# Kernel optimization log

Measured on AMD Instinct MI355X. Metric: run time of the kernel, lower is better.

## Reference

```python
import jax, jax.numpy as jnp
import numpy as np

DIM = 128      # token feature dim
HEADS = 4
HEAD_DIM = DIM // HEADS
H = 512
W = 512
NSP = 4096     # n_spixels = H*W/scale
TEMP = DIM ** (-0.5)   # NOTE: original scales by full-dim ** -0.5
NEG = -9.0e15
EPS = 1e-12    # torch F.normalize eps


def setup_inputs() -> dict:
    key = jax.random.key(0)
    k1, k2, k3, k4 = jax.random.split(key, 4)
    return {
        "spf": jax.random.normal(k1, (DIM, NSP), jnp.float32),
        "segments": jax.random.randint(k2, (H, W), 0, NSP, jnp.int32),
        "w_qkv": jax.random.normal(k3, (DIM, 3 * DIM), jnp.float32) / np.sqrt(DIM),
        "w_out": jax.random.normal(k4, (DIM, DIM), jnp.float32) / np.sqrt(DIM),
        "b_out": jnp.zeros((DIM,), jnp.float32),
    }


def build_adjacency(seg, n_sp):
    """Vectorized version of get_A: for every 2x2 window (i in [0,h-3], j in [0,w-3])
    connect the max and min superpixel labels; zero the diagonal."""
    a = seg[:-2, :-2]
    b = seg[:-2, 1:-1]
    c = seg[1:-1, :-2]
    d = seg[1:-1, 1:-1]
    mx = jnp.maximum(jnp.maximum(a, b), jnp.maximum(c, d)).ravel()
    mn = jnp.minimum(jnp.minimum(a, b), jnp.minimum(c, d)).ravel()
    A = jnp.zeros((n_sp, n_sp), jnp.float32)
    A = A.at[mx, mn].set(1.0)
    A = A.at[mn, mx].set(1.0)
    # fill_diagonal(A, 0) (also removes windows where max == min)
    A = A * (1.0 - jnp.eye(n_sp, dtype=jnp.float32))
    return A


def _l2norm(t):
    n = jnp.sqrt(jnp.sum(t * t, axis=-1, keepdims=True))
    return t / jnp.maximum(n, EPS)


def reference(spf, segments, w_qkv, w_out, b_out):
    A = build_adjacency(segments, NSP)                      # [n, n]
    x = spf.T                                               # [n, dim]
    qkv = x @ w_qkv                                         # [n, 3*dim]
    q, k, v = jnp.split(qkv, 3, axis=-1)
    split = lambda t: t.reshape(NSP, HEADS, HEAD_DIM).transpose(1, 0, 2)  # [h, n, d]
    q, k, v = split(q), split(k), split(v)
    q = _l2norm(q)
    k = _l2norm(k)
    # Original masks per-head scores, then keeps only head 0's attention
    # (attn[0][0]) and broadcasts it over all heads' v. We compute only
    # head 0's scores (mathematically identical output).
    scores = (q[0] @ k[0].T) * TEMP                         # [n, n] cosine scores
    scores = jnp.where(A > 0, scores, NEG)
    eye = jnp.eye(NSP, dtype=bool)
    scores = jnp.where(eye, 1.0, scores)                    # np.fill_diagonal(attn, 1)
    attn = jax.nn.softmax(scores, axis=-1)                  # [n, n]
    out = jnp.einsum('nm,hmd->hnd', attn, v)                # shared attn over heads
    out = out.transpose(1, 0, 2).reshape(NSP, DIM)          # [n, dim]
    out = out @ w_out + b_out                               # to_out Linear
    # map_sp2p: scatter superpixel features back to pixel grid (hard assignment)
    pix = out[segments]                                     # [H, W, dim]
    return pix.transpose(2, 0, 1)[None]                     # [1, dim, H, W]
```

## Files before the change

### kernel.cpp

```cpp
#include <hip/hip_runtime.h>

#define NSP 4096
#define HW 512
#define TEMP 0.08838834764831845f
#define MAXE 640
#define ADJ_BLOCKS 1017
#define GEMM_BLOCKS 256

__global__ void __launch_bounds__(256) adj_qkv(
    const int* __restrict__ seg, unsigned int* __restrict__ mask,
    const float* __restrict__ spf, const float* __restrict__ wqkv,
    const float* __restrict__ wout,
    float* __restrict__ Q0, float* __restrict__ K0, float* __restrict__ V) {
    __shared__ float xs[128][16];
    __shared__ float vrs[16][128];
    int t = threadIdx.x;
    if (blockIdx.x < ADJ_BLOCKS) {
        int idx = blockIdx.x * 256 + t;
        if (idx >= 510 * 510) return;
        int i = idx / 510, j = idx - i * 510;
        const int* r = seg + i * HW + j;
        int a = r[0], b = r[1], c = r[HW], d = r[HW + 1];
        int mx = max(max(a, b), max(c, d));
        int mn = min(min(a, b), min(c, d));
        if (mx == mn) return;
        atomicOr(&mask[mx * 128 + (mn >> 5)], 1u << (mn & 31));
        atomicOr(&mask[mn * 128 + (mx >> 5)], 1u << (mx & 31));
        return;
    }
    int nbase = (blockIdx.x - ADJ_BLOCKS) * 16;
#pragma unroll
    for (int i = 0; i < 8; ++i) {
        int idx = t + 256 * i;
        int d = idx >> 4, nn = idx & 15;
        xs[d][nn] = spf[d * NSP + nbase + nn];
    }
    __syncthreads();
    int n = t >> 4, k = t & 15;
    int ng = nbase + n;
    const float* wq = (k < 8) ? (wqkv + k * 4) : (wqkv + 96 + k * 4);
    const float* wv1 = wqkv + 256 + 4 * k;
    const float* wv2 = wqkv + 256 + 64 + 4 * k;
    float4 a0 = {0.f,0.f,0.f,0.f}, a1 = {0.f,0.f,0.f,0.f}, a2 = {0.f,0.f,0.f,0.f};
#pragma unroll 4
    for (int d = 0; d < 128; ++d) {
        float x = xs[d][n];
        float4 wa = *(const float4*)(wq  + d * 384);
        float4 wb = *(const float4*)(wv1 + d * 384);
        float4 wc = *(const float4*)(wv2 + d * 384);
        a0.x += x * wa.x; a0.y += x * wa.y; a0.z += x * wa.z; a0.w += x * wa.w;
        a1.x += x * wb.x; a1.y += x * wb.y; a1.z += x * wb.z; a1.w += x * wb.w;
        a2.x += x * wc.x; a2.y += x * wc.y; a2.z += x * wc.z; a2.w += x * wc.w;
    }
    float s = a0.x * a0.x + a0.y * a0.y + a0.z * a0.z + a0.w * a0.w;
    s += __shfl_xor(s, 1);
    s += __shfl_xor(s, 2);
    s += __shfl_xor(s, 4);
    float inv = 1.0f / fmaxf(sqrtf(s), 1e-12f);
    a0.x *= inv; a0.y *= inv; a0.z *= inv; a0.w *= inv;
    float* qk = (k < 8) ? (Q0 + ng * 32 + k * 4) : (K0 + ng * 32 + (k - 8) * 4);
    *(float4*)qk = a0;
    *(float4*)&vrs[n][4 * k] = a1;
    *(float4*)&vrs[n][64 + 4 * k] = a2;
    __syncthreads();
    float4 c1 = {0.f,0.f,0.f,0.f}, c2 = {0.f,0.f,0.f,0.f};
#pragma unroll 4
    for (int d = 0; d < 128; ++d) {
        float v = vrs[n][d];
        float4 w1 = *(const float4*)(wout + d * 128 + 4 * k);
        float4 w2 = *(const float4*)(wout + d * 128 + 64 + 4 * k);
        c1.x += v * w1.x; c1.y += v * w1.y; c1.z += v * w1.z; c1.w += v * w1.w;
        c2.x += v * w2.x; c2.y += v * w2.y; c2.z += v * w2.z; c2.w += v * w2.w;
    }
    *(float4*)(V + ng * 128 + 4 * k) = c1;
    *(float4*)(V + ng * 128 + 64 + 4 * k) = c2;
}

__global__ void __launch_bounds__(256) sparse_attn(
    const unsigned int* __restrict__ mask, const float* __restrict__ Q0,
    const float* __restrict__ K0, const float* __restrict__ V,
    const float* __restrict__ bout, float* __restrict__ fin) {
    __shared__ unsigned int words[4][128];
    __shared__ int   pfx[4][128];
    __shared__ int   midx[4][MAXE];
    __shared__ float wts[4][MAXE];
    __shared__ float q0s[4][32];
    int t = threadIdx.x, lane = t & 63, w = t >> 6;
    int n = blockIdx.x * 4 + w;

    uint2 mw = ((const uint2*)(mask + n * 128))[lane];
    ((uint2*)words[w])[lane] = mw;
    int pc1 = __popc(mw.y);
    int p = __popc(mw.x) + pc1;
#pragma unroll
    for (int off = 1; off < 64; off <<= 1) {
        int y = __shfl_up(p, off);
        if (lane >= off) p += y;
    }
    pfx[w][2 * lane + 1] = p;
    pfx[w][2 * lane]     = p - pc1;
    int E = min(__shfl(p, 63), MAXE);
    if (lane < 32) q0s[w][lane] = Q0[n * 32 + lane];
    __syncthreads();

    for (int e = lane; e < E; e += 64) {
        int lo = 0, hi = 127;
        while (lo < hi) { int mid = (lo + hi) >> 1; if (pfx[w][mid] > e) hi = mid; else lo = mid + 1; }
        int base = lo ? pfx[w][lo - 1] : 0;
        int r = e - base;
        unsigned int x = words[w][lo];
        for (int i = 0; i < r; ++i) x &= x - 1;
        int m = lo * 32 + (__ffs(x) - 1);
        const float4* kp = (const float4*)(K0 + m * 32);
        float s = 0.f;
#pragma unroll
        for (int i = 0; i < 8; ++i) {
            float4 kv = kp[i];
            s += q0s[w][4 * i + 0] * kv.x + q0s[w][4 * i + 1] * kv.y +
                 q0s[w][4 * i + 2] * kv.z + q0s[w][4 * i + 3] * kv.w;
        }
        wts[w][e]  = __expf(s * TEMP - 1.0f);
        midx[w][e] = m;
    }
    __syncthreads();

    int cgc = lane & 31, eg = lane >> 5;
    const float4* V4 = (const float4*)V;
    float4 acc = {0.f,0.f,0.f,0.f};
    float wp = 0.f;
    int e = eg;
    for (; e + 2 < E; e += 4) {
        float wa = wts[w][e];     int ma = midx[w][e];
        float wb = wts[w][e + 2]; int mb = midx[w][e + 2];
        float4 va = V4[ma * 32 + cgc];
        float4 vb = V4[mb * 32 + cgc];
        acc.x += wa * va.x + wb * vb.x;
        acc.y += wa * va.y + wb * vb.y;
        acc.z += wa * va.z + wb * vb.z;
        acc.w += wa * va.w + wb * vb.w;
        wp += wa + wb;
    }
    for (; e < E; e += 2) {
        float wt = wts[w][e];
        float4 v = V4[midx[w][e] * 32 + cgc];
        acc.x += wt * v.x; acc.y += wt * v.y; acc.z += wt * v.z; acc.w += wt * v.w;
        wp += wt;
    }
    acc.x += __shfl_xor(acc.x, 32);
    acc.y += __shfl_xor(acc.y, 32);
    acc.z += __shfl_xor(acc.z, 32);
    acc.w += __shfl_xor(acc.w, 32);
    wp    += __shfl_xor(wp, 32);
    if (lane < 32) {
        float4 vd = V4[n * 32 + cgc];
        float4 bb = ((const float4*)bout)[cgc];
        float inv = 1.0f / (1.0f + wp);
        float4 o;
        o.x = (acc.x + vd.x) * inv + bb.x;
        o.y = (acc.y + vd.y) * inv + bb.y;
        o.z = (acc.z + vd.z) * inv + bb.z;
        o.w = (acc.w + vd.w) * inv + bb.w;
        ((float4*)fin)[n * 32 + cgc] = o;
    }
}

#define GOUT_PIX 256
#define GOUT_CH  32
__global__ void __launch_bounds__(256) gather_out(
    const float* __restrict__ fin, const int* __restrict__ seg,
    float* __restrict__ out) {
    __shared__ __align__(16) float tile[GOUT_CH][260];
    __shared__ int sseg[GOUT_PIX];
    int t = threadIdx.x;
    int pixbase = (blockIdx.x >> 2) * GOUT_PIX;
    int cbase = (blockIdx.x & 3) * GOUT_CH;

    sseg[t] = seg[pixbase + t];
    __syncthreads();

    const float4* f4 = (const float4*)fin;
    int c8 = t & 7;
    int pp = t >> 3;
#pragma unroll
    for (int i = 0; i < 8; ++i) {
        int p = pp + 32 * i;
        float4 v = f4[sseg[p] * 32 + (cbase >> 2) + c8];
        tile[4 * c8 + 0][p] = v.x;
        tile[4 * c8 + 1][p] = v.y;
        tile[4 * c8 + 2][p] = v.z;
        tile[4 * c8 + 3][p] = v.w;
    }
    __syncthreads();

    int wv = t >> 6, lane = t & 63;
#pragma unroll
    for (int s = 0; s < 8; ++s) {
        int ch = wv * 8 + s;
        float4 v = *(const float4*)&tile[ch][4 * lane];
        *(float4*)(out + (size_t)(cbase + ch) * (HW * HW) + pixbase + 4 * lane) = v;
    }
}

extern "C" void kernel_launch(void* const* d_in, const int* in_sizes, int n_in,
                              void* d_out, int out_size, void* d_ws, size_t ws_size,
                              hipStream_t stream) {
    const float* spf  = (const float*)d_in[0];
    const int*   seg  = (const int*)d_in[1];
    const float* wqkv = (const float*)d_in[2];
    const float* wout = (const float*)d_in[3];
    const float* bout = (const float*)d_in[4];
    float* out = (float*)d_out;

    char* ws = (char*)d_ws;
    unsigned int* mask = (unsigned int*)ws;
    float* Q0  = (float*)(ws + 0x200000);
    float* K0  = (float*)(ws + 0x280000);
    float* V   = (float*)(ws + 0x300000);
    float* fin = (float*)(ws + 0x500000);

    hipMemsetAsync(mask, 0, 2u << 20, stream);
    hipLaunchKernelGGL(adj_qkv, dim3(ADJ_BLOCKS + GEMM_BLOCKS), dim3(256), 0, stream,
                       seg, mask, spf, wqkv, wout, Q0, K0, V);
    hipLaunchKernelGGL(sparse_attn, dim3(1024), dim3(256), 0, stream,
                       mask, Q0, K0, V, bout, fin);
    hipLaunchKernelGGL(gather_out, dim3((HW * HW) / GOUT_PIX * 4), dim3(256), 0, stream,
                       fin, seg, out);
}
```

Before: 230.3 us.

## Use one block per superpixel row with atomic edge compaction in sparse attention

Sparse attention now launches one 128-thread block per row instead of one wavefront per row. Each thread scans a single mask word and appends its neighbour indices through an LDS atomic counter, which replaces the prefix-sum, binary-search and bit-peeling edge enumeration. Score computation and V accumulation are spread over 128 threads, and the partial sums are reduced through shared memory. Edge order becomes nondeterministic, so floating-point summation order can vary between runs, and the extra block syncs add per-row overhead.

Result: no change. 226.1 us (-1.8%).

```diff
diff --git a/kernel.cpp b/kernel.cpp
--- a/kernel.cpp
+++ b/kernel.cpp
@@ -76,91 +76,84 @@
     *(float4*)(V + ng * 128 + 64 + 4 * k) = c2;
 }
 
-__global__ void __launch_bounds__(256) sparse_attn(
+__global__ void __launch_bounds__(128) sparse_attn(
     const unsigned int* __restrict__ mask, const float* __restrict__ Q0,
     const float* __restrict__ K0, const float* __restrict__ V,
     const float* __restrict__ bout, float* __restrict__ fin) {
-    __shared__ unsigned int words[4][128];
-    __shared__ int   pfx[4][128];
-    __shared__ int   midx[4][MAXE];
-    __shared__ float wts[4][MAXE];
-    __shared__ float q0s[4][32];
-    int t = threadIdx.x, lane = t & 63, w = t >> 6;
-    int n = blockIdx.x * 4 + w;
-
-    uint2 mw = ((const uint2*)(mask + n * 128))[lane];
-    ((uint2*)words[w])[lane] = mw;
-    int pc1 = __popc(mw.y);
-    int p = __popc(mw.x) + pc1;
-#pragma unroll
-    for (int off = 1; off < 64; off <<= 1) {
-        int y = __shfl_up(p, off);
-        if (lane >= off) p += y;
-    }
-    pfx[w][2 * lane + 1] = p;
-    pfx[w][2 * lane]     = p - pc1;
-    int E = min(__shfl(p, 63), MAXE);
-    if (lane < 32) q0s[w][lane] = Q0[n * 32 + lane];
-    __syncthreads();
-
-    for (int e = lane; e < E; e += 64) {
-        int lo = 0, hi = 127;
-        while (lo < hi) { int mid = (lo + hi) >> 1; if (pfx[w][mid] > e) hi = mid; else lo = mid + 1; }
-        int base = lo ? pfx[w][lo - 1] : 0;
-        int r = e - base;
-        unsigned int x = words[w][lo];
-        for (int i = 0; i < r; ++i) x &= x - 1;
-        int m = lo * 32 + (__ffs(x) - 1);
+    int n = blockIdx.x;
+    int t = threadIdx.x;
+    __shared__ int   midx[MAXE];
+    __shared__ float wts[MAXE];
+    __shared__ float q0s[32];
+    __shared__ float4 redv[4][32];
+    __shared__ float  redw[4];
+    __shared__ int ecnt;
+
+    unsigned int w = mask[n * 128 + t];
+    if (t == 0) ecnt = 0;
+    if (t < 32) q0s[t] = Q0[n * 32 + t];
+    __syncthreads();
+
+    while (w) {
+        int b = __ffs(w) - 1;
+        w &= w - 1;
+        int pos = atomicAdd(&ecnt, 1);
+        if (pos < MAXE) midx[pos] = t * 32 + b;
+    }
+    __syncthreads();
+    int E = min(ecnt, MAXE);
+
+    for (int e = t; e < E; e += 128) {
+        int m = midx[e];
         const float4* kp = (const float4*)(K0 + m * 32);
         float s = 0.f;
 #pragma unroll
         for (int i = 0; i < 8; ++i) {
             float4 kv = kp[i];
-            s += q0s[w][4 * i + 0] * kv.x + q0s[w][4 * i + 1] * kv.y +
-                 q0s[w][4 * i + 2] * kv.z + q0s[w][4 * i + 3] * kv.w;
+            s += q0s[4 * i + 0] * kv.x + q0s[4 * i + 1] * kv.y +
+                 q0s[4 * i + 2] * kv.z + q0s[4 * i + 3] * kv.w;
         }
-        wts[w][e]  = __expf(s * TEMP - 1.0f);
-        midx[w][e] = m;
-    }
-    __syncthreads();
-
-    int cgc = lane & 31, eg = lane >> 5;
+        wts[e] = __expf(s * TEMP - 1.0f);
+    }
+    __syncthreads();
+
+    int cg = t & 31, eg = t >> 5;
     const float4* V4 = (const float4*)V;
-    float4 acc = {0.f,0.f,0.f,0.f};
+    float4 acc = {0.f, 0.f, 0.f, 0.f};
     float wp = 0.f;
     int e = eg;
-    for (; e + 2 < E; e += 4) {
-        float wa = wts[w][e];     int ma = midx[w][e];
-        float wb = wts[w][e + 2]; int mb = midx[w][e + 2];
-        float4 va = V4[ma * 32 + cgc];
-        float4 vb = V4[mb * 32 + cgc];
+    for (; e + 4 < E; e += 8) {
+        float wa = wts[e];     int ma = midx[e];
+        float wb = wts[e + 4]; int mb = midx[e + 4];
+        float4 va = V4[ma * 32 + cg];
+        float4 vb = V4[mb * 32 + cg];
         acc.x += wa * va.x + wb * vb.x;
         acc.y += wa * va.y + wb * vb.y;
         acc.z += wa * va.z + wb * vb.z;
         acc.w += wa * va.w + wb * vb.w;
         wp += wa + wb;
     }
-    for (; e < E; e += 2) {
-        float wt = wts[w][e];
-        float4 v = V4[midx[w][e] * 32 + cgc];
+    for (; e < E; e += 4) {
+        float wt = wts[e];
+        float4 v = V4[midx[e] * 32 + cg];
         acc.x += wt * v.x; acc.y += wt * v.y; acc.z += wt * v.z; acc.w += wt * v.w;
         wp += wt;
     }
-    acc.x += __shfl_xor(acc.x, 32);
-    acc.y += __shfl_xor(acc.y, 32);
-    acc.z += __shfl_xor(acc.z, 32);
-    acc.w += __shfl_xor(acc.w, 32);
-    wp    += __shfl_xor(wp, 32);
-    if (lane < 32) {
-        float4 vd = V4[n * 32 + cgc];
-        float4 bb = ((const float4*)bout)[cgc];
-        float inv = 1.0f / (1.0f + wp);
+    redv[eg][cg] = acc;
+    if (cg == 0) redw[eg] = wp;
+    __syncthreads();
+    if (t < 32) {
+        float4 a0 = redv[0][t], a1 = redv[1][t], a2 = redv[2][t], a3 = redv[3][t];
+        float ws = 1.0f + redw[0] + redw[1] + redw[2] + redw[3];
+        float4 vd = V4[n * 32 + t];
+        float4 bb = ((const float4*)bout)[t];
+        float inv = 1.0f / ws;
         float4 o;
-        o.x = (acc.x + vd.x) * inv + bb.x;
-        o.y = (acc.y + vd.y) * inv + bb.y;
-        o.z = (acc.z + vd.z) * inv + bb.z;
-        o.w = (acc.w + vd.w) * inv + bb.w;
-        ((float4*)fin)[n * 32 + cgc] = o;
+        o.x = (a0.x + a1.x + a2.x + a3.x + vd.x) * inv + bb.x;
+        o.y = (a0.y + a1.y + a2.y + a3.y + vd.y) * inv + bb.y;
+        o.z = (a0.z + a1.z + a2.z + a3.z + vd.z) * inv + bb.z;
+        o.w = (a0.w + a1.w + a2.w + a3.w + vd.w) * inv + bb.w;
+        ((float4*)fin)[n * 32 + t] = o;
     }
 }
 
@@ -221,7 +214,7 @@
     hipMemsetAsync(mask, 0, 2u << 20, stream);
     hipLaunchKernelGGL(adj_qkv, dim3(ADJ_BLOCKS + GEMM_BLOCKS), dim3(256), 0, stream,
                        seg, mask, spf, wqkv, wout, Q0, K0, V);
-    hipLaunchKernelGGL(sparse_attn, dim3(1024), dim3(256), 0, stream,
+    hipLaunchKernelGGL(sparse_attn, dim3(4096), dim3(128), 0, stream,
                        mask, Q0, K0, V, bout, fin);
     hipLaunchKernelGGL(gather_out, dim3((HW * HW) / GOUT_PIX * 4), dim3(256), 0, stream,
                        fin, seg, out);
```
